# Kernel optimization log

Measured on AMD Instinct MI355X. Metric: run time of the kernel, lower is better.

The kernel has to match this reference:

```python
import jax, jax.numpy as jnp
import numpy as np

NUM_GROUPS = 32
EPS = 1e-5


def group_norm(x, w, b):
    # x: [B,C,H,W], 32 groups
    B, C, H, W = x.shape
    xg = x.reshape(B, NUM_GROUPS, C // NUM_GROUPS, H, W)
    mean = xg.mean(axis=(2, 3, 4), keepdims=True)
    var = xg.var(axis=(2, 3, 4), keepdims=True)
    xn = ((xg - mean) * jax.lax.rsqrt(var + EPS)).reshape(B, C, H, W)
    return xn * w[None, :, None, None] + b[None, :, None, None]


def conv1x1(x, w, b):
    # x: [B,C,H,W], w: [O,C], b: [O]
    return jnp.einsum('bchw,oc->bohw', x, w) + b[None, :, None, None]


def setup_inputs() -> dict:
    key = jax.random.key(0)
    ks = jax.random.split(key, 7)
    B, C, H, W = 16, 512, 32, 32
    x = jax.random.normal(ks[0], (B, C, H, W), dtype=jnp.float32)
    gn_w = jnp.ones((C,), dtype=jnp.float32)
    gn_b = jnp.zeros((C,), dtype=jnp.float32)
    s = 1.0 / np.sqrt(C)
    qkv_w = jax.random.normal(ks[1], (3 * C, C), dtype=jnp.float32) * s
    qkv_b = jnp.zeros((3 * C,), dtype=jnp.float32)
    proj_w = jax.random.normal(ks[2], (C, C), dtype=jnp.float32) * s
    proj_b = jnp.zeros((C,), dtype=jnp.float32)
    return {"x": x, "gn_w": gn_w, "gn_b": gn_b, "qkv_w": qkv_w,
            "qkv_b": qkv_b, "proj_w": proj_w, "proj_b": proj_b}


def reference(x, gn_w, gn_b, qkv_w, qkv_b, proj_w, proj_b):
    B, C, H, W = x.shape
    qkv = conv1x1(group_norm(x, gn_w, gn_b), qkv_w, qkv_b)
    q, k, v = jnp.split(qkv, 3, axis=1)
    scale = (C // 8) ** (-0.5)
    # attn: [B, h, w, H, W]
    attn = jnp.einsum('bchw,bcHW->bhwHW', q * scale, k)
    # NOTE: faithful to original torch code: softmax over the LAST axis only
    attn = jax.nn.softmax(attn, axis=-1)
    out = jnp.einsum('bhwHW,bcHW->bchw', attn, v)
    return x + conv1x1(out, proj_w, proj_b)
```

## Files before the change

### kernel.cpp

```cpp
#include <hip/hip_runtime.h>
#include <hip/hip_bf16.h>

#define B_    16
#define C_    512
#define S_    1024
#define NGRP  32
#define CPG   16

typedef __attribute__((ext_vector_type(8))) short  short8;
typedef __attribute__((ext_vector_type(4))) short  short4v;
typedef __attribute__((ext_vector_type(4))) float  floatx4;

__device__ __forceinline__ unsigned short f2bf(float f) {
    __hip_bfloat16 h = __float2bfloat16(f);
    unsigned short u;
    __builtin_memcpy(&u, &h, 2);
    return u;
}

__global__ __launch_bounds__(256)
void gn_fused_kernel(const float* __restrict__ x, const float* __restrict__ w,
                     const float* __restrict__ bias, __hip_bfloat16* __restrict__ xnT) {
    int bg = blockIdx.x;
    int b = bg >> 5, g = bg & 31;
    const float4* xp = (const float4*)(x + (size_t)bg * (CPG * S_));
    int tid = threadIdx.x;

    float4 vv[16];
    float s = 0.f, ss = 0.f;
#pragma unroll
    for (int r = 0; r < 16; ++r) {
        float4 v = xp[r * 256 + tid];
        vv[r] = v;
        s  += v.x + v.y + v.z + v.w;
        ss += v.x*v.x + v.y*v.y + v.z*v.z + v.w*v.w;
    }
    for (int off = 32; off > 0; off >>= 1) {
        s  += __shfl_down(s, off);
        ss += __shfl_down(ss, off);
    }
    __shared__ float red[2][4];
    __shared__ float msh[2];
    int wid = tid >> 6, lane = tid & 63;
    if (lane == 0) { red[0][wid] = s; red[1][wid] = ss; }
    __syncthreads();
    if (tid == 0) {
        float a = 0.f, c = 0.f;
        for (int i = 0; i < 4; ++i) { a += red[0][i]; c += red[1][i]; }
        float mean = a / (float)(CPG * S_);
        float var  = c / (float)(CPG * S_) - mean * mean;
        msh[0] = mean;
        msh[1] = rsqrtf(var + 1e-5f);
    }
    __syncthreads();
    float mean = msh[0], inv = msh[1];

    float sc[16], sh[16];
#pragma unroll
    for (int c = 0; c < 16; ++c) {
        float wc = w[g * 16 + c];
        sc[c] = inv * wc;
        sh[c] = bias[g * 16 + c] - mean * inv * wc;
    }

#pragma unroll
    for (int kk = 0; kk < 4; ++kk) {
        unsigned short outp[16];
#pragma unroll
        for (int c = 0; c < 16; ++c) {
            float v = (kk == 0) ? vv[c].x : (kk == 1) ? vv[c].y : (kk == 2) ? vv[c].z : vv[c].w;
            outp[c] = f2bf(v * sc[c] + sh[c]);
        }
        int srow = 4 * tid + kk;
        unsigned short* dst = (unsigned short*)xnT + ((size_t)(b * S_ + srow) * C_ + g * 16);
        *(short8*)dst       = *(short8*)outp;
        *(short8*)(dst + 8) = *(short8*)(outp + 8);
    }
}

__global__ __launch_bounds__(256)
void prep_kernel(const float* __restrict__ qkv_w, const float* __restrict__ proj_w,
                 const float* __restrict__ qkv_b,
                 unsigned short* __restrict__ bufX,
                 unsigned short* __restrict__ bufY,
                 float* __restrict__ bqWk, float* __restrict__ biasvp)
{
    int blk = blockIdx.x;
    int tid = threadIdx.x;
    if (blk < 192) {
        __shared__ float T[64][65];
        int mat = blk >> 6, tile = blk & 63;
        int r0 = (tile >> 3) * 64, c0 = (tile & 7) * 64;
        const float* src; unsigned short* dst;
        if (mat == 0)      { src = qkv_w + 512 * 512;  dst = bufX; }
        else if (mat == 1) { src = qkv_w;              dst = bufY; }
        else               { src = qkv_w + 1024 * 512; dst = bufY + 262144; }
#pragma unroll
        for (int rr = 0; rr < 4; ++rr) {
            int sr = rr * 16 + (tid >> 4);
            int sc = (tid & 15) * 4;
            float4 v = *(const float4*)(src + (size_t)(c0 + sr) * 512 + r0 + sc);
            T[sc][sr] = v.x; T[sc + 1][sr] = v.y; T[sc + 2][sr] = v.z; T[sc + 3][sr] = v.w;
        }
        __syncthreads();
#pragma unroll
        for (int rr = 0; rr < 4; ++rr) {
            int dr = rr * 16 + (tid >> 4);
            int dc = (tid & 15) * 4;
            short4v o;
            o[0] = (short)f2bf(T[dr][dc]);     o[1] = (short)f2bf(T[dr][dc + 1]);
            o[2] = (short)f2bf(T[dr][dc + 2]); o[3] = (short)f2bf(T[dr][dc + 3]);
            *(short4v*)(dst + (size_t)(r0 + dr) * 512 + c0 + dc) = o;
        }
    } else if (blk < 256) {
        unsigned short* wp = bufX + 262144;
#pragma unroll
        for (int t = 0; t < 4; ++t) {
            int i = (blk - 192) * 4096 + t * 1024 + tid * 4;
            float4 v = *(const float4*)(proj_w + i);
            short4v o;
            o[0] = (short)f2bf(v.x); o[1] = (short)f2bf(v.y);
            o[2] = (short)f2bf(v.z); o[3] = (short)f2bf(v.w);
            *(short4v*)(wp + i) = o;
        }
    } else if (blk < 264) {
        int sub = blk - 256;
        int j = (sub & 1) * 256 + tid;
        int o0 = (sub >> 1) * 128;
        float acc = 0.f;
#pragma unroll 8
        for (int oo = 0; oo < 128; ++oo) {
            int o = o0 + oo;
            acc += qkv_b[o] * qkv_w[(size_t)(512 + o) * 512 + j];
        }
        atomicAdd(&bqWk[j], acc);
    } else {
        int wv = tid >> 6, lane = tid & 63;
        int c = (blk - 264) * 4 + wv;
        float s = 0.f;
#pragma unroll
        for (int t = 0; t < 8; ++t)
            s += proj_w[(size_t)c * 512 + t * 64 + lane] * qkv_b[1024 + t * 64 + lane];
        for (int off = 32; off > 0; off >>= 1) s += __shfl_down(s, off);
        if (lane == 0) biasvp[c] = s;
    }
}

template<int BIAS_MODE, bool OUT_BF16, bool RESID, bool SWIZ, int KTOT>
__global__ __launch_bounds__(256)
void mfma_gemm(const unsigned short* __restrict__ A, const unsigned short* __restrict__ Bm,
               const float* __restrict__ bias, const float* __restrict__ resid,
               void* __restrict__ Yv,
               int lda, int ldb, int ldy,
               size_t sA, size_t sB, size_t sY, size_t sR, float alpha,
               int ntsh, int nxsh)
{
    __shared__ unsigned short As[2 * 128 * 32];
    __shared__ unsigned short Bs[2 * 128 * 32];
    int bx, by, bz;
    if (SWIZ) {
        int lin = blockIdx.x;
        int xcd = lin & 7, sup = lin >> 3;
        bz = xcd + ((sup >> ntsh) << 3);
        int tile = sup & ((1 << ntsh) - 1);
        bx = tile & ((1 << nxsh) - 1);
        by = tile >> nxsh;
    } else { bx = blockIdx.x; by = blockIdx.y; bz = blockIdx.z; }

    const unsigned short* Ab = A  + (size_t)bz * sA;
    const unsigned short* Bb = Bm + (size_t)bz * sB;
    const int tid = threadIdx.x, wave = tid >> 6, lane = tid & 63;
    const int m0 = by * 128, n0 = bx * 128;
    const int wr = wave >> 1, wc = wave & 1, lr = lane & 15, kq = lane >> 4;
    const int row0 = tid >> 2, kc0 = (tid & 3) << 3;

    floatx4 acc[4][4] = {};

    for (int k0 = 0; k0 < KTOT; k0 += 64) {
        __syncthreads();
#pragma unroll
        for (int kk = 0; kk < 2; ++kk) {
#pragma unroll
            for (int r = 0; r < 2; ++r) {
                const unsigned short* ga = Ab + (size_t)(m0 + r * 64 + row0) * lda + k0 + kk * 32 + kc0;
                __builtin_amdgcn_global_load_lds(
                    (const __attribute__((address_space(1))) void*)ga,
                    (__attribute__((address_space(3))) void*)(As + kk * 4096 + (r * 256 + wave * 64) * 8),
                    16, 0, 0);
                const unsigned short* gb = Bb + (size_t)(n0 + r * 64 + row0) * ldb + k0 + kk * 32 + kc0;
                __builtin_amdgcn_global_load_lds(
                    (const __attribute__((address_space(1))) void*)gb,
                    (__attribute__((address_space(3))) void*)(Bs + kk * 4096 + (r * 256 + wave * 64) * 8),
                    16, 0, 0);
            }
        }
        __syncthreads();

#pragma unroll
        for (int kk = 0; kk < 2; ++kk) {
            short8 af[4], bfr[4];
#pragma unroll
            for (int i = 0; i < 4; ++i)
                af[i] = *(const short8*)&As[kk * 4096 + (wr * 64 + i * 16 + lr) * 32 + kq * 8];
#pragma unroll
            for (int j = 0; j < 4; ++j)
                bfr[j] = *(const short8*)&Bs[kk * 4096 + (wc * 64 + j * 16 + lr) * 32 + kq * 8];
#pragma unroll
            for (int i = 0; i < 4; ++i)
#pragma unroll
                for (int j = 0; j < 4; ++j)
                    acc[i][j] = __builtin_amdgcn_mfma_f32_16x16x32_bf16(af[i], bfr[j], acc[i][j], 0, 0, 0);
        }
    }

    const size_t ybase = (size_t)bz * sY;
    const size_t rbase = (size_t)bz * sR;
#pragma unroll
    for (int i = 0; i < 4; ++i) {
#pragma unroll
        for (int r = 0; r < 4; ++r) {
            int m = m0 + wr * 64 + i * 16 + kq * 4 + r;
            float bm = (BIAS_MODE == 1) ? bias[m] : 0.f;
#pragma unroll
            for (int j = 0; j < 4; ++j) {
                int n = n0 + wc * 64 + j * 16 + lr;
                float vv = acc[i][j][r] * alpha + bm;
                if (BIAS_MODE == 2) vv += bias[n];
                if (RESID) vv += resid[rbase + (size_t)m * ldy + n];
                if (OUT_BF16)
                    ((__hip_bfloat16*)Yv)[ybase + (size_t)m * ldy + n] = __float2bfloat16(vv);
                else
                    ((float*)Yv)[ybase + (size_t)m * ldy + n] = vv;
            }
        }
    }
}

__global__ __launch_bounds__(256)
void scores_softmax_kernel(const unsigned short* __restrict__ A,
                           const unsigned short* __restrict__ Bm,
                           unsigned short* __restrict__ P)
{
    __shared__ unsigned short smem[128 * 136];
    unsigned short* As = smem;
    unsigned short* Bs = smem + 8192;

    int lin = blockIdx.x;
    int xcd = lin & 7, sup = lin >> 3;
    int bz = xcd + ((sup >> 6) << 3);
    int tile = sup & 63;
    int bx = tile & 7, by = tile >> 3;

    const size_t sAB = (size_t)S_ * 512;
    const unsigned short* Ab = A  + (size_t)bz * sAB;
    const unsigned short* Bb = Bm + (size_t)bz * sAB;
    const int tid = threadIdx.x, wave = tid >> 6, lane = tid & 63;
    const int m0 = by * 128, n0 = bx * 128;
    const int wr = wave >> 1, wc = wave & 1, lr = lane & 15, kq = lane >> 4;
    const int row0 = tid >> 2, kc0 = (tid & 3) << 3;

    floatx4 acc[4][4] = {};

    for (int k0 = 0; k0 < 512; k0 += 64) {
        __syncthreads();
#pragma unroll
        for (int kk = 0; kk < 2; ++kk) {
#pragma unroll
            for (int r = 0; r < 2; ++r) {
                const unsigned short* ga = Ab + (size_t)(m0 + r * 64 + row0) * 512 + k0 + kk * 32 + kc0;
                __builtin_amdgcn_global_load_lds(
                    (const __attribute__((address_space(1))) void*)ga,
                    (__attribute__((address_space(3))) void*)(As + kk * 4096 + (r * 256 + wave * 64) * 8),
                    16, 0, 0);
                const unsigned short* gb = Bb + (size_t)(n0 + r * 64 + row0) * 512 + k0 + kk * 32 + kc0;
                __builtin_amdgcn_global_load_lds(
                    (const __attribute__((address_space(1))) void*)gb,
                    (__attribute__((address_space(3))) void*)(Bs + kk * 4096 + (r * 256 + wave * 64) * 8),
                    16, 0, 0);
            }
        }
        __syncthreads();

#pragma unroll
        for (int kk = 0; kk < 2; ++kk) {
            short8 af[4], bfr[4];
#pragma unroll
            for (int i = 0; i < 4; ++i)
                af[i] = *(const short8*)&As[kk * 4096 + (wr * 64 + i * 16 + lr) * 32 + kq * 8];
#pragma unroll
            for (int j = 0; j < 4; ++j)
                bfr[j] = *(const short8*)&Bs[kk * 4096 + (wc * 64 + j * 16 + lr) * 32 + kq * 8];
#pragma unroll
            for (int i = 0; i < 4; ++i)
#pragma unroll
                for (int j = 0; j < 4; ++j)
                    acc[i][j] = __builtin_amdgcn_mfma_f32_16x16x32_bf16(af[i], bfr[j], acc[i][j], 0, 0, 0);
        }
    }

    __syncthreads();

#pragma unroll
    for (int j = 0; j < 4; ++j) {
        int sq_l = wc * 64 + j * 16 + lr;
#pragma unroll
        for (int h = 0; h < 2; ++h) {
            float v0[4], v1[4];
            float mx = -1e30f;
#pragma unroll
            for (int r = 0; r < 4; ++r) {
                v0[r] = acc[2 * h][j][r]     * 0.125f;
                v1[r] = acc[2 * h + 1][j][r] * 0.125f;
                mx = fmaxf(mx, fmaxf(v0[r], v1[r]));
            }
            mx = fmaxf(mx, __shfl_xor(mx, 16));
            mx = fmaxf(mx, __shfl_xor(mx, 32));
            float sm = 0.f;
#pragma unroll
            for (int r = 0; r < 4; ++r) {
                v0[r] = __expf(v0[r] - mx);
                v1[r] = __expf(v1[r] - mx);
                sm += v0[r] + v1[r];
            }
            sm += __shfl_xor(sm, 16);
            sm += __shfl_xor(sm, 32);
            float inv = 1.f / sm;
            short4v p0, p1;
#pragma unroll
            for (int r = 0; r < 4; ++r) {
                p0[r] = (short)f2bf(v0[r] * inv);
                p1[r] = (short)f2bf(v1[r] * inv);
            }
            int key0 = wr * 64 + 32 * h + kq * 4;
            *(short4v*)&smem[sq_l * 136 + key0]      = p0;
            *(short4v*)&smem[sq_l * 136 + key0 + 16] = p1;
        }
    }
    __syncthreads();

    int row = tid >> 1, half = tid & 1;
    const unsigned short* src = smem + row * 136 + half * 64;
    size_t gbase = (size_t)bz * ((size_t)S_ * S_) + (size_t)(n0 + row) * 1024 + m0 + half * 64;
#pragma unroll
    for (int t = 0; t < 8; ++t) {
        short8 v = *(const short8*)(src + t * 8);
        *(short8*)(P + gbase + t * 8) = v;
    }
}

extern "C" void kernel_launch(void* const* d_in, const int* in_sizes, int n_in,
                              void* d_out, int out_size, void* d_ws, size_t ws_size,
                              hipStream_t stream) {
    const float* x     = (const float*)d_in[0];
    const float* gn_w  = (const float*)d_in[1];
    const float* gn_b  = (const float*)d_in[2];
    const float* qkv_w = (const float*)d_in[3];
    const float* qkv_b = (const float*)d_in[4];
    const float* pr_w  = (const float*)d_in[5];
    const float* pr_b  = (const float*)d_in[6];
    float* out = (float*)d_out;

    char* w = (char*)d_ws;
    __hip_bfloat16* xnT  = (__hip_bfloat16*)w;
    __hip_bfloat16* u    = (__hip_bfloat16*)(w + (16u << 20));
    __hip_bfloat16* Vp   = (__hip_bfloat16*)(w + (32u << 20));
    __hip_bfloat16* P    = (__hip_bfloat16*)(w + (48u << 20));
    unsigned short* bufX = (unsigned short*)(w + (80u << 20));
    unsigned short* bufY = (unsigned short*)(w + (81u << 20));
    unsigned short* bufZ = (unsigned short*)(w + (82u << 20));
    float*          bqWk = (float*)(w + (83u << 20));
    float*          bvp  = (float*)(w + (83u << 20) + 4096);

    hipMemsetAsync(bqWk, 0, 512 * sizeof(float), stream);

    prep_kernel<<<392, 256, 0, stream>>>(qkv_w, pr_w, qkv_b, bufX, bufY, bqWk, bvp);

    gn_fused_kernel<<<B_ * NGRP, 256, 0, stream>>>(x, gn_w, gn_b, xnT);

    mfma_gemm<0, true, false, false, 512><<<dim3(4, 4, 2), 256, 0, stream>>>(
        bufX, bufY, nullptr, nullptr, bufZ,
        512, 512, 512, 262144, 262144, 262144, 0, 1.f, 0, 0);

    mfma_gemm<2, true, false, false, 512><<<dim3(4, 128, 1), 256, 0, stream>>>(
        (const unsigned short*)xnT, bufZ, bqWk, nullptr, u,
        512, 512, 512, 0, 0, 0, 0, 1.f, 0, 0);

    mfma_gemm<1, true, false, true, 512><<<512, 256, 0, stream>>>(
        bufZ + 262144, (const unsigned short*)xnT, bvp, nullptr, Vp,
        512, 512, 1024, 0, (size_t)S_ * 512, (size_t)512 * S_, 0, 1.f, 5, 3);

    scores_softmax_kernel<<<1024, 256, 0, stream>>>(
        (const unsigned short*)xnT, (const unsigned short*)u, (unsigned short*)P);

    mfma_gemm<1, false, true, true, 1024><<<512, 256, 0, stream>>>(
        (const unsigned short*)Vp, (const unsigned short*)P, pr_b, x, out,
        1024, 1024, 1024, (size_t)512 * S_, (size_t)S_ * S_, (size_t)512 * S_,
        (size_t)512 * S_, 1.f, 5, 3);
}
```

Baseline: 217.0 us.

## Rewrite scores+softmax kernel as 256x256 tile, 8-wave pipelined, swizzled LDS

Replaces the 128x128-tile scores/softmax kernel with a 256x256-tile version using 512 threads, double-buffered global-to-LDS loads interleaved with MFMA phases, XOR-swizzled LDS layout, and priority raising around MFMA blocks. The aim is to overlap loads with compute, raise data reuse per tile and avoid LDS bank conflicts. It uses 128KB of LDS per block, limiting occupancy to one block per CU, and launches only 256 blocks, which may underfill the GPU.

Result: faster. 209.6 us (-3.4%).

```diff
diff --git a/kernel.cpp b/kernel.cpp
--- a/kernel.cpp
+++ b/kernel.cpp
@@ -236,75 +236,141 @@
     }
 }
 
-__global__ __launch_bounds__(256)
-void scores_softmax_kernel(const unsigned short* __restrict__ A,
-                           const unsigned short* __restrict__ Bm,
-                           unsigned short* __restrict__ P)
+__global__ __launch_bounds__(512)
+void scores_softmax8(const unsigned short* __restrict__ A,
+                     const unsigned short* __restrict__ Bm,
+                     unsigned short* __restrict__ P)
 {
-    __shared__ unsigned short smem[128 * 136];
-    unsigned short* As = smem;
-    unsigned short* Bs = smem + 8192;
-
-    int lin = blockIdx.x;
-    int xcd = lin & 7, sup = lin >> 3;
-    int bz = xcd + ((sup >> 6) << 3);
-    int tile = sup & 63;
-    int bx = tile & 7, by = tile >> 3;
+    __shared__ __align__(16) unsigned short lds[65536];
+    char* asb = (char*)lds;
+    char* bsb = (char*)lds + 65536;
+
+    const int bid = blockIdx.x;
+    const int bz = bid >> 4, t16 = bid & 15;
+    const int by = t16 >> 2, bx = t16 & 3;
+    const int m0 = by << 8, n0 = bx << 8;
 
     const size_t sAB = (size_t)S_ * 512;
     const unsigned short* Ab = A  + (size_t)bz * sAB;
     const unsigned short* Bb = Bm + (size_t)bz * sAB;
+
     const int tid = threadIdx.x, wave = tid >> 6, lane = tid & 63;
-    const int m0 = by * 128, n0 = bx * 128;
-    const int wr = wave >> 1, wc = wave & 1, lr = lane & 15, kq = lane >> 4;
-    const int row0 = tid >> 2, kc0 = (tid & 3) << 3;
-
-    floatx4 acc[4][4] = {};
-
-    for (int k0 = 0; k0 < 512; k0 += 64) {
-        __syncthreads();
-#pragma unroll
-        for (int kk = 0; kk < 2; ++kk) {
-#pragma unroll
-            for (int r = 0; r < 2; ++r) {
-                const unsigned short* ga = Ab + (size_t)(m0 + r * 64 + row0) * 512 + k0 + kk * 32 + kc0;
-                __builtin_amdgcn_global_load_lds(
-                    (const __attribute__((address_space(1))) void*)ga,
-                    (__attribute__((address_space(3))) void*)(As + kk * 4096 + (r * 256 + wave * 64) * 8),
-                    16, 0, 0);
-                const unsigned short* gb = Bb + (size_t)(n0 + r * 64 + row0) * 512 + k0 + kk * 32 + kc0;
-                __builtin_amdgcn_global_load_lds(
-                    (const __attribute__((address_space(1))) void*)gb,
-                    (__attribute__((address_space(3))) void*)(Bs + kk * 4096 + (r * 256 + wave * 64) * 8),
-                    16, 0, 0);
-            }
-        }
-        __syncthreads();
-
-#pragma unroll
-        for (int kk = 0; kk < 2; ++kk) {
-            short8 af[4], bfr[4];
-#pragma unroll
-            for (int i = 0; i < 4; ++i)
-                af[i] = *(const short8*)&As[kk * 4096 + (wr * 64 + i * 16 + lr) * 32 + kq * 8];
-#pragma unroll
-            for (int j = 0; j < 4; ++j)
-                bfr[j] = *(const short8*)&Bs[kk * 4096 + (wc * 64 + j * 16 + lr) * 32 + kq * 8];
-#pragma unroll
-            for (int i = 0; i < 4; ++i)
-#pragma unroll
-                for (int j = 0; j < 4; ++j)
-                    acc[i][j] = __builtin_amdgcn_mfma_f32_16x16x32_bf16(af[i], bfr[j], acc[i][j], 0, 0, 0);
-        }
-    }
-
-    __syncthreads();
+    const int wr = wave >> 2, wc = wave & 3;
+    const int lr = lane & 15, kq = lane >> 4;
+    const int swz = (lr & 7) << 4;
+
+    floatx4 acc[8][4] = {};
+    short8 aF[4][2], bF[2][2][2];
+
+    auto stage = [&](const unsigned short* __restrict__ G, int row0, int t,
+                     char* base, int buf, int half) {
+#pragma unroll
+        for (int c = 0; c < 2; ++c) {
+            int x = c * 8192 + tid * 16;
+            int row = x >> 7;
+            int colb = (x & 127) ^ ((row & 7) << 4);
+            const unsigned short* ga = G + (((size_t)(row0 + row)) << 9) + (t << 6) + (colb >> 1);
+            char* ldst = base + buf * 32768 + half * 16384 + c * 8192 + wave * 1024;
+            __builtin_amdgcn_global_load_lds(
+                (const __attribute__((address_space(1))) void*)ga,
+                (__attribute__((address_space(3))) void*)ldst, 16, 0, 0);
+        }
+    };
+    auto rdA = [&](int buf, int mh, int ii, int kk) {
+        int byte = buf * 32768 + wr * 16384 + (mh * 64 + ii * 16 + lr) * 128
+                 + ((kk * 64 + kq * 16) ^ swz);
+        return *(const short8*)(asb + byte);
+    };
+    auto rdB = [&](int buf, int nh, int jj, int kk) {
+        int trow = wc * 64 + (nh * 2 + jj) * 16 + lr;
+        int byte = buf * 32768 + (trow >> 7) * 16384 + (trow & 127) * 128
+                 + ((kk * 64 + kq * 16) ^ swz);
+        return *(const short8*)(bsb + byte);
+    };
+
+    stage(Ab, m0,       0, asb, 0, 0);
+    stage(Bb, n0,       0, bsb, 0, 0);
+    stage(Bb, n0 + 128, 0, bsb, 0, 1);
+    stage(Ab, m0 + 128, 0, asb, 0, 1);
+    stage(Ab, m0,       1, asb, 1, 0);
+    stage(Bb, n0,       1, bsb, 1, 0);
+    stage(Bb, n0 + 128, 1, bsb, 1, 1);
+    asm volatile("s_waitcnt vmcnt(6)" ::: "memory");
+    __builtin_amdgcn_s_barrier();
+
+    for (int t = 0; t < 8; ++t) {
+        const int buf = t & 1;
+#pragma unroll
+        for (int ii = 0; ii < 4; ++ii) { aF[ii][0] = rdA(buf, 0, ii, 0); aF[ii][1] = rdA(buf, 0, ii, 1); }
+#pragma unroll
+        for (int jj = 0; jj < 2; ++jj) { bF[0][jj][0] = rdB(buf, 0, jj, 0); bF[0][jj][1] = rdB(buf, 0, jj, 1); }
+        if (t < 7) stage(Ab, m0 + 128, t + 1, asb, (t + 1) & 1, 1);
+        __builtin_amdgcn_s_barrier();
+        asm volatile("s_waitcnt lgkmcnt(0)" ::: "memory");
+        __builtin_amdgcn_s_setprio(1);
+#pragma unroll
+        for (int ii = 0; ii < 4; ++ii)
+#pragma unroll
+            for (int jj = 0; jj < 2; ++jj)
+#pragma unroll
+                for (int kk = 0; kk < 2; ++kk)
+                    acc[ii][jj] = __builtin_amdgcn_mfma_f32_16x16x32_bf16(aF[ii][kk], bF[0][jj][kk], acc[ii][jj], 0, 0, 0);
+        __builtin_amdgcn_s_setprio(0);
+        __builtin_amdgcn_s_barrier();
+#pragma unroll
+        for (int jj = 0; jj < 2; ++jj) { bF[1][jj][0] = rdB(buf, 1, jj, 0); bF[1][jj][1] = rdB(buf, 1, jj, 1); }
+        __builtin_amdgcn_s_barrier();
+        asm volatile("s_waitcnt lgkmcnt(0)" ::: "memory");
+        __builtin_amdgcn_s_setprio(1);
+#pragma unroll
+        for (int ii = 0; ii < 4; ++ii)
+#pragma unroll
+            for (int jj = 0; jj < 2; ++jj)
+#pragma unroll
+                for (int kk = 0; kk < 2; ++kk)
+                    acc[ii][2 + jj] = __builtin_amdgcn_mfma_f32_16x16x32_bf16(aF[ii][kk], bF[1][jj][kk], acc[ii][2 + jj], 0, 0, 0);
+        __builtin_amdgcn_s_setprio(0);
+        __builtin_amdgcn_s_barrier();
+#pragma unroll
+        for (int ii = 0; ii < 4; ++ii) { aF[ii][0] = rdA(buf, 1, ii, 0); aF[ii][1] = rdA(buf, 1, ii, 1); }
+        if (t < 6) stage(Bb, n0, t + 2, bsb, buf, 0);
+        __builtin_amdgcn_s_barrier();
+        asm volatile("s_waitcnt lgkmcnt(0)" ::: "memory");
+        __builtin_amdgcn_s_setprio(1);
+#pragma unroll
+        for (int ii = 0; ii < 4; ++ii)
+#pragma unroll
+            for (int jj = 0; jj < 2; ++jj)
+#pragma unroll
+                for (int kk = 0; kk < 2; ++kk)
+                    acc[4 + ii][2 + jj] = __builtin_amdgcn_mfma_f32_16x16x32_bf16(aF[ii][kk], bF[1][jj][kk], acc[4 + ii][2 + jj], 0, 0, 0);
+        __builtin_amdgcn_s_setprio(0);
+        __builtin_amdgcn_s_barrier();
+        if (t < 6) {
+            stage(Ab, m0,       t + 2, asb, buf, 0);
+            stage(Bb, n0 + 128, t + 2, bsb, buf, 1);
+        }
+        __builtin_amdgcn_s_setprio(1);
+#pragma unroll
+        for (int ii = 0; ii < 4; ++ii)
+#pragma unroll
+            for (int jj = 0; jj < 2; ++jj)
+#pragma unroll
+                for (int kk = 0; kk < 2; ++kk)
+                    acc[4 + ii][jj] = __builtin_amdgcn_mfma_f32_16x16x32_bf16(aF[ii][kk], bF[0][jj][kk], acc[4 + ii][jj], 0, 0, 0);
+        __builtin_amdgcn_s_setprio(0);
+        if (t < 6) { asm volatile("s_waitcnt vmcnt(6)" ::: "memory"); }
+        else       { asm volatile("s_waitcnt vmcnt(0)" ::: "memory"); }
+        __builtin_amdgcn_s_barrier();
+    }
 
 #pragma unroll
     for (int j = 0; j < 4; ++j) {
-        int sq_l = wc * 64 + j * 16 + lr;
-#pragma unroll
-        for (int h = 0; h < 2; ++h) {
+        int sqc = wc * 64 + j * 16 + lr;
+        int srow = sqc * 512;
+        int sxor = (sqc & 7) << 4;
+#pragma unroll
+        for (int h = 0; h < 4; ++h) {
             float v0[4], v1[4];
             float mx = -1e30f;
 #pragma unroll
@@ -331,20 +397,20 @@
                 p0[r] = (short)f2bf(v0[r] * inv);
                 p1[r] = (short)f2bf(v1[r] * inv);
             }
-            int key0 = wr * 64 + 32 * h + kq * 4;
-            *(short4v*)&smem[sq_l * 136 + key0]      = p0;
-            *(short4v*)&smem[sq_l * 136 + key0 + 16] = p1;
+            int kb = (wr * 128 + h * 32 + kq * 4) * 2;
+            *(short4v*)(asb + ((srow + kb) ^ sxor))      = p0;
+            *(short4v*)(asb + ((srow + kb + 32) ^ sxor)) = p1;
         }
     }
     __syncthreads();
 
-    int row = tid >> 1, half = tid & 1;
-    const unsigned short* src = smem + row * 136 + half * 64;
-    size_t gbase = (size_t)bz * ((size_t)S_ * S_) + (size_t)(n0 + row) * 1024 + m0 + half * 64;
-#pragma unroll
-    for (int t = 0; t < 8; ++t) {
-        short8 v = *(const short8*)(src + t * 8);
-        *(short8*)(P + gbase + t * 8) = v;
+    const size_t pbase = ((size_t)bz << 20) + (size_t)n0 * 1024 + m0;
+#pragma unroll
+    for (int it = 0; it < 16; ++it) {
+        int row = wave * 32 + it * 2 + (lane >> 5);
+        int colb = (lane & 31) << 4;
+        short8 v = *(const short8*)(asb + ((row * 512 + colb) ^ ((row & 7) << 4)));
+        *(short8*)(P + pbase + (size_t)row * 1024 + (colb >> 1)) = v;
     }
 }
 
@@ -389,7 +455,7 @@
         bufZ + 262144, (const unsigned short*)xnT, bvp, nullptr, Vp,
         512, 512, 1024, 0, (size_t)S_ * 512, (size_t)512 * S_, 0, 1.f, 5, 3);
 
-    scores_softmax_kernel<<<1024, 256, 0, stream>>>(
+    scores_softmax8<<<256, 512, 0, stream>>>(
         (const unsigned short*)xnT, (const unsigned short*)u, (unsigned short*)P);
 
     mfma_gemm<1, false, true, true, 1024><<<512, 256, 0, stream>>>(
```
